# Kernel tuning notes

Hardware: AMD Instinct MI355X
Metric: run time of the kernel (lower is better)

Reference implementation:

```python
import jax, jax.numpy as jnp
import numpy as np
import math

D_MODEL = 1024
H = 16
D_K = D_MODEL // H
D_FF = 4096
NEG = -1e9


def layer_norm(x, alpha, bias):
    # Faithful to source: mean over last dim, UNBIASED std (torch.std default),
    # eps defined in source but never used in forward.
    mean = jnp.mean(x, axis=-1, keepdims=True)
    std = jnp.std(x, axis=-1, ddof=1, keepdims=True)
    return (x - mean) / std * alpha + bias


def mha(x, mask, w_q, w_k, w_v, w_o):
    B, S, D = x.shape
    q = (x @ w_q.T).reshape(B, S, H, D_K)
    k = (x @ w_k.T).reshape(B, S, H, D_K)
    v = (x @ w_v.T).reshape(B, S, H, D_K)
    scores = jnp.einsum('bqhd,bkhd->bhqk', q, k) / math.sqrt(D_K)
    scores = jnp.where(mask, NEG, scores)
    attn = jax.nn.softmax(scores, axis=-1)
    out = jnp.einsum('bhqk,bkhd->bqhd', attn, v).reshape(B, S, D)
    return out @ w_o.T


def setup_inputs() -> dict:
    key = jax.random.key(0)
    ks = jax.random.split(key, 16)
    B, S = 4, 2048
    s = 0.02
    return {
        'x': jax.random.normal(ks[0], (B, S, D_MODEL), jnp.float32),
        'w_q': jax.random.normal(ks[1], (D_MODEL, D_MODEL), jnp.float32) * s,
        'w_k': jax.random.normal(ks[2], (D_MODEL, D_MODEL), jnp.float32) * s,
        'w_v': jax.random.normal(ks[3], (D_MODEL, D_MODEL), jnp.float32) * s,
        'w_o': jax.random.normal(ks[4], (D_MODEL, D_MODEL), jnp.float32) * s,
        'l1_w': jax.random.normal(ks[5], (D_FF, D_MODEL), jnp.float32) * s,
        'l1_b': jnp.zeros((D_FF,), jnp.float32),
        'l2_w': jax.random.normal(ks[6], (D_MODEL, D_FF), jnp.float32) * s,
        'l2_b': jnp.zeros((D_MODEL,), jnp.float32),
        'norm1_a': jnp.ones((D_MODEL,), jnp.float32),
        'norm1_b': jnp.zeros((D_MODEL,), jnp.float32),
        'norm2_a': jnp.ones((D_MODEL,), jnp.float32),
        'norm2_b': jnp.zeros((D_MODEL,), jnp.float32),
        'normf_a': jnp.ones((D_MODEL,), jnp.float32),
        'normf_b': jnp.zeros((D_MODEL,), jnp.float32),
        'mask': jax.random.randint(ks[7], (B, 1, 1, S), 0, 2) == 1,
    }


def reference(x, w_q, w_k, w_v, w_o, l1_w, l1_b, l2_w, l2_b,
              norm1_a, norm1_b, norm2_a, norm2_b, normf_a, normf_b, mask):
    # residual 1: pre-norm self-attention (dropout is identity at eval)
    x = x + mha(layer_norm(x, norm1_a, norm1_b), mask, w_q, w_k, w_v, w_o)
    # residual 2: pre-norm FFN
    h = layer_norm(x, norm2_a, norm2_b)
    ff = jax.nn.relu(h @ l1_w.T + l1_b) @ l2_w.T + l2_b
    x = x + ff
    return layer_norm(x, normf_a, normf_b)
```

## Files before the change

kernel.cpp:

```cpp
#include <hip/hip_runtime.h>
#include <hip/hip_bf16.h>


typedef __bf16 bf16x8 __attribute__((ext_vector_type(8)));
typedef float f32x4 __attribute__((ext_vector_type(4)));
typedef unsigned short u16x8 __attribute__((ext_vector_type(8)));
using bf16 = __hip_bfloat16;

__device__ __forceinline__ f32x4 mfma16(bf16x8 a, bf16x8 b, f32x4 c) {
  return __builtin_amdgcn_mfma_f32_16x16x32_bf16(a, b, c, 0, 0, 0);
}

__device__ __forceinline__ int swz(int row, int blk) {
  return row * 64 + ((blk ^ (row & 7)) << 3);
}

__device__ __forceinline__ void stage_tile64(unsigned short* lds,
                                             const bf16* g, int ld, int rows) {
  const int lane = threadIdx.x & 63, wid = threadIdx.x >> 6;
  const int r8 = lane >> 3, blk = lane & 7;
  const bf16* gl = g + (size_t)r8 * ld + ((blk ^ r8) << 3);
  const int passes = rows >> 3;
  for (int p = wid; p < passes; p += 4) {
    __builtin_amdgcn_global_load_lds(
        (const __attribute__((address_space(1))) void*)(gl + (size_t)(p * 8) * ld),
        (__attribute__((address_space(3))) void*)(lds + p * 512),
        16, 0, 0);
  }
}

__device__ __forceinline__ short bfb(float x) {
  return (short)__hip_bfloat16_raw(__float2bfloat16(x)).x;
}

__global__ __launch_bounds__(256) void cvt_k(const float* __restrict__ s,
                                             bf16* __restrict__ d, int n) {
  const int i = (blockIdx.x * 256 + threadIdx.x) * 4;
  if (i + 3 < n) {
    const float4 v = *reinterpret_cast<const float4*>(s + i);
    ushort4 o;
    o.x = (unsigned short)bfb(v.x);
    o.y = (unsigned short)bfb(v.y);
    o.z = (unsigned short)bfb(v.z);
    o.w = (unsigned short)bfb(v.w);
    *reinterpret_cast<ushort4*>(d + i) = o;
  }
}

template <bool OUT_F32>
__global__ __launch_bounds__(256) void layernorm_k(const float* __restrict__ in,
                                                   const float* __restrict__ gamma,
                                                   const float* __restrict__ beta,
                                                   void* __restrict__ out) {
  __shared__ float red[8];
  const int row = blockIdx.x, t = threadIdx.x;
  const float4 vv = reinterpret_cast<const float4*>(in + (size_t)row * 1024)[t];
  const float x0 = vv.x, x1 = vv.y, x2 = vv.z, x3 = vv.w;
  float s = x0 + x1 + x2 + x3;
#pragma unroll
  for (int off = 32; off; off >>= 1) s += __shfl_down(s, off);
  if ((t & 63) == 0) red[t >> 6] = s;
  __syncthreads();
  const float mean = (red[0] + red[1] + red[2] + red[3]) * (1.0f / 1024.0f);
  const float d0 = x0 - mean, d1 = x1 - mean, d2 = x2 - mean, d3 = x3 - mean;
  float sq = d0 * d0 + d1 * d1 + d2 * d2 + d3 * d3;
#pragma unroll
  for (int off = 32; off; off >>= 1) sq += __shfl_down(sq, off);
  if ((t & 63) == 0) red[4 + (t >> 6)] = sq;
  __syncthreads();
  const float var =
      fmaxf((red[4] + red[5] + red[6] + red[7]) * (1.0f / 1023.0f), 1e-20f);
  const float rstd = rsqrtf(var);
  const float4 ga = reinterpret_cast<const float4*>(gamma)[t];
  const float4 be = reinterpret_cast<const float4*>(beta)[t];
  const float y0 = d0 * rstd * ga.x + be.x;
  const float y1 = d1 * rstd * ga.y + be.y;
  const float y2 = d2 * rstd * ga.z + be.z;
  const float y3 = d3 * rstd * ga.w + be.w;
  if (OUT_F32) {
    reinterpret_cast<float4*>((float*)out + (size_t)row * 1024)[t] =
        make_float4(y0, y1, y2, y3);
  } else {
    ushort4 o;
    o.x = (unsigned short)bfb(y0);
    o.y = (unsigned short)bfb(y1);
    o.z = (unsigned short)bfb(y2);
    o.w = (unsigned short)bfb(y3);
    reinterpret_cast<ushort4*>((bf16*)out + (size_t)row * 1024)[t] = o;
  }
}

template <bool HAS_BIAS, bool RELU, bool HAS_RES, bool OUT_F32>
__global__ __launch_bounds__(256) void gemm_bt(const bf16* __restrict__ A,
                                               const bf16* __restrict__ W,
                                               const float* __restrict__ bias,
                                               const float* __restrict__ resid,
                                               void* __restrict__ out,
                                               int M, int N, int K,
                                               int lda, int ldw) {
  __shared__ __align__(16) unsigned short As[128 * 64];
  __shared__ __align__(16) unsigned short Bs[128 * 64];
  const int lane = threadIdx.x & 63, wid = threadIdx.x >> 6;
  const int n16 = lane & 15, quad = lane >> 4;
  const int wm = (wid >> 1) * 64, wn = (wid & 1) * 64;
  const int tm = blockIdx.x * 128, tn = blockIdx.y * 128;
  f32x4 acc[4][4] = {};
  for (int k0 = 0; k0 < K; k0 += 64) {
    stage_tile64(As, A + (size_t)tm * lda + k0, lda, 128);
    stage_tile64(Bs, W + (size_t)tn * ldw + k0, ldw, 128);
    __syncthreads();
#pragma unroll
    for (int kk = 0; kk < 64; kk += 32) {
      bf16x8 af[4], bw[4];
#pragma unroll
      for (int i = 0; i < 4; ++i)
        af[i] = *reinterpret_cast<const bf16x8*>(
            &As[swz(wm + i * 16 + n16, (kk >> 3) + quad)]);
#pragma unroll
      for (int j = 0; j < 4; ++j)
        bw[j] = *reinterpret_cast<const bf16x8*>(
            &Bs[swz(wn + j * 16 + n16, (kk >> 3) + quad)]);
#pragma unroll
      for (int i = 0; i < 4; ++i)
#pragma unroll
        for (int j = 0; j < 4; ++j) acc[i][j] = mfma16(af[i], bw[j], acc[i][j]);
    }
    __syncthreads();
  }
#pragma unroll
  for (int i = 0; i < 4; ++i) {
#pragma unroll
    for (int j = 0; j < 4; ++j) {
      const int n = tn + wn + j * 16 + n16;
      const float bv = HAS_BIAS ? bias[n] : 0.0f;
#pragma unroll
      for (int r = 0; r < 4; ++r) {
        const int m = tm + wm + i * 16 + quad * 4 + r;
        float vv = acc[i][j][r] + bv;
        if (RELU) vv = fmaxf(vv, 0.0f);
        if (HAS_RES) vv += resid[(size_t)m * N + n];
        if (OUT_F32)
          ((float*)out)[(size_t)m * N + n] = vv;
        else
          ((bf16*)out)[(size_t)m * N + n] = __float2bfloat16(vv);
      }
    }
  }
}

__global__ void detect_mask_k(const unsigned int* __restrict__ m,
                              int* __restrict__ flag) {
  __shared__ int s;
  if (threadIdx.x == 0) s = 0;
  __syncthreads();
  unsigned int acc = 0;
  for (int i = threadIdx.x; i < 512; i += 256) acc |= m[i] & 0xFFFFFF00u;
  if (acc) atomicOr(&s, 1);
  __syncthreads();
  if (threadIdx.x == 0) *flag = s;
}

__global__ __launch_bounds__(256) void prep_mask_k(const int* __restrict__ m,
                                                   const int* __restrict__ flag,
                                                   float* __restrict__ mf,
                                                   int n) {
  const int i = blockIdx.x * 256 + threadIdx.x;
  if (i < n) {
    const int v = (*flag) ? (int)((const unsigned char*)m)[i] : m[i];
    mf[i] = v ? -1e9f : 0.0f;
  }
}

__global__ __launch_bounds__(256) void attn_k(const bf16* __restrict__ q,
                                              const bf16* __restrict__ kmat,
                                              const bf16* __restrict__ v,
                                              const float* __restrict__ maskf,
                                              bf16* __restrict__ out, int BHN) {
  __shared__ __align__(16) unsigned short Ks[64 * 64];
  __shared__ __align__(16) unsigned short Vs[64 * 72];
  const int lane = threadIdx.x & 63, wid = threadIdx.x >> 6;
  const int n16 = lane & 15, quad = lane >> 4;
  const int bid = blockIdx.x;
  const int bh = bid % BHN, qb = bid / BHN;
  const int b = bh >> 4, h = bh & 15;
  const size_t bhoff = (size_t)b * 2048 * 1024 + h * 64;
  const float* mfb = maskf + b * 2048;
  const int qrow0 = qb * 128 + wid * 32;

  bf16x8 qf[2][2];
#pragma unroll
  for (int g = 0; g < 2; ++g) {
    const bf16* qp = q + bhoff + (size_t)(qrow0 + g * 16 + n16) * 1024 + quad * 8;
    qf[g][0] = *reinterpret_cast<const bf16x8*>(qp);
    qf[g][1] = *reinterpret_cast<const bf16x8*>(qp + 32);
  }
  bf16x8 ones;
#pragma unroll
  for (int e = 0; e < 8; ++e) ones[e] = (__bf16)1.0f;
  f32x4 oacc[2][4] = {};
  f32x4 lacc[2] = {};
  const int prow = ((n16 >> 2) << 3) + (n16 & 3);

  for (int kt = 0; kt < 2048; kt += 64) {
    stage_tile64(Ks, kmat + bhoff + (size_t)kt * 1024, 1024, 64);
    {
      const int key = lane, dc = wid * 16;
      const bf16* vp = v + bhoff + (size_t)(kt + key) * 1024 + dc;
      const u16x8 a = *reinterpret_cast<const u16x8*>(vp);
      const u16x8 bq = *reinterpret_cast<const u16x8*>(vp + 8);
#pragma unroll
      for (int e = 0; e < 8; ++e) {
        Vs[(dc + e) * 72 + key] = a[e];
        Vs[(dc + 8 + e) * 72 + key] = bq[e];
      }
    }
    __syncthreads();
#pragma unroll
    for (int sub = 0; sub < 2; ++sub) {
      const int kb = sub * 32;
      bf16x8 aflo[2], afhi[2];
#pragma unroll
      for (int st = 0; st < 2; ++st) {
        const int row = kb + prow + st * 4;
        aflo[st] = *reinterpret_cast<const bf16x8*>(&Ks[swz(row, quad)]);
        afhi[st] = *reinterpret_cast<const bf16x8*>(&Ks[swz(row, 4 + quad)]);
      }
      f32x4 z[2][2];
#pragma unroll
      for (int g = 0; g < 2; ++g)
#pragma unroll
        for (int st = 0; st < 2; ++st) {
          f32x4 zz = {};
          zz = mfma16(aflo[st], qf[g][0], zz);
          zz = mfma16(afhi[st], qf[g][1], zz);
          z[g][st] = zz;
        }
      const float4 m0 =
          *reinterpret_cast<const float4*>(mfb + kt + kb + quad * 8);
      const float4 m1 =
          *reinterpret_cast<const float4*>(mfb + kt + kb + quad * 8 + 4);
      bf16x8 vf[4];
#pragma unroll
      for (int j = 0; j < 4; ++j)
        vf[j] = *reinterpret_cast<const bf16x8*>(
            &Vs[(j * 16 + n16) * 72 + kb + quad * 8]);
#pragma unroll
      for (int g = 0; g < 2; ++g) {
        bf16x8 pf;
#pragma unroll
        for (int r = 0; r < 4; ++r) {
          const float e0 =
              __expf(fmaf(z[g][0][r], 0.125f, ((const float*)&m0)[r]));
          const float e1 =
              __expf(fmaf(z[g][1][r], 0.125f, ((const float*)&m1)[r]));
          pf[r] = (__bf16)e0;
          pf[4 + r] = (__bf16)e1;
        }
#pragma unroll
        for (int j = 0; j < 4; ++j) oacc[g][j] = mfma16(pf, vf[j], oacc[g][j]);
        lacc[g] = mfma16(pf, ones, lacc[g]);
      }
    }
    __syncthreads();
  }
#pragma unroll
  for (int g = 0; g < 2; ++g) {
#pragma unroll
    for (int r = 0; r < 4; ++r) {
      const float lr = 1.0f / fmaxf(lacc[g][r], 1e-20f);
      bf16* op = out + bhoff + (size_t)(qrow0 + g * 16 + quad * 4 + r) * 1024;
#pragma unroll
      for (int j = 0; j < 4; ++j)
        op[j * 16 + n16] = __float2bfloat16(oacc[g][j][r] * lr);
    }
  }
}

extern "C" void kernel_launch(void* const* d_in, const int* in_sizes, int n_in,
                              void* d_out, int out_size, void* d_ws,
                              size_t ws_size, hipStream_t stream) {
  const float* x    = (const float*)d_in[0];
  const float* w_q  = (const float*)d_in[1];
  const float* w_k  = (const float*)d_in[2];
  const float* w_v  = (const float*)d_in[3];
  const float* w_o  = (const float*)d_in[4];
  const float* l1_w = (const float*)d_in[5];
  const float* l1_b = (const float*)d_in[6];
  const float* l2_w = (const float*)d_in[7];
  const float* l2_b = (const float*)d_in[8];
  const float* n1a  = (const float*)d_in[9];
  const float* n1b  = (const float*)d_in[10];
  const float* n2a  = (const float*)d_in[11];
  const float* n2b  = (const float*)d_in[12];
  const float* nfa  = (const float*)d_in[13];
  const float* nfb  = (const float*)d_in[14];
  const int* mask   = (const int*)d_in[15];

  const int D = 1024, FF = 4096;
  const int M = in_sizes[0] / D;

  const size_t MB = 1024ull * 1024ull;
  if (ws_size < 121 * MB) return;
  char* w = (char*)d_ws;
  bf16* WQ  = (bf16*)(w + 0 * MB);
  bf16* WK  = (bf16*)(w + 2 * MB);
  bf16* WV  = (bf16*)(w + 4 * MB);
  bf16* WO  = (bf16*)(w + 6 * MB);
  bf16* L1W = (bf16*)(w + 8 * MB);
  bf16* L2W = (bf16*)(w + 16 * MB);
  bf16* LN1 = (bf16*)(w + 24 * MB);
  bf16* Qb  = (bf16*)(w + 40 * MB);
  bf16* Kb  = (bf16*)(w + 56 * MB);
  bf16* Vb  = (bf16*)(w + 72 * MB);
  bf16* ATT = LN1;
  bf16* HLN = Qb;
  bf16* FF1 = Kb;
  float* X1 = (float*)(w + 88 * MB);
  int* FLAG = (int*)(w + 120 * MB);
  float* MASKF = (float*)(w + 120 * MB + 256);

  const dim3 blk(256);
  cvt_k<<<dim3(D * D / 1024), blk, 0, stream>>>(w_q, WQ, D * D);
  cvt_k<<<dim3(D * D / 1024), blk, 0, stream>>>(w_k, WK, D * D);
  cvt_k<<<dim3(D * D / 1024), blk, 0, stream>>>(w_v, WV, D * D);
  cvt_k<<<dim3(D * D / 1024), blk, 0, stream>>>(w_o, WO, D * D);
  cvt_k<<<dim3(FF * D / 1024), blk, 0, stream>>>(l1_w, L1W, FF * D);
  cvt_k<<<dim3(FF * D / 1024), blk, 0, stream>>>(l2_w, L2W, FF * D);
  detect_mask_k<<<1, blk, 0, stream>>>((const unsigned int*)mask, FLAG);
  prep_mask_k<<<dim3((M + 255) / 256), blk, 0, stream>>>(mask, FLAG, MASKF, M);

  layernorm_k<false><<<M, blk, 0, stream>>>(x, n1a, n1b, LN1);
  gemm_bt<false, false, false, false><<<dim3(M / 128, D / 128), blk, 0, stream>>>(
      LN1, WQ, nullptr, nullptr, Qb, M, D, D, D, D);
  gemm_bt<false, false, false, false><<<dim3(M / 128, D / 128), blk, 0, stream>>>(
      LN1, WK, nullptr, nullptr, Kb, M, D, D, D, D);
  gemm_bt<false, false, false, false><<<dim3(M / 128, D / 128), blk, 0, stream>>>(
      LN1, WV, nullptr, nullptr, Vb, M, D, D, D, D);
  const int BHN = (M / 2048) * 16;
  attn_k<<<dim3((M / 128) * 16), blk, 0, stream>>>(Qb, Kb, Vb, MASKF, ATT, BHN);
  gemm_bt<false, false, true, true><<<dim3(M / 128, D / 128), blk, 0, stream>>>(
      ATT, WO, nullptr, x, X1, M, D, D, D, D);
  layernorm_k<false><<<M, blk, 0, stream>>>(X1, n2a, n2b, HLN);
  for (int c = 0; c < 2; ++c) {
    gemm_bt<true, true, false, false>
        <<<dim3(M / 128, 2048 / 128), blk, 0, stream>>>(
            HLN, L1W + (size_t)c * 2048 * D, l1_b + c * 2048, nullptr, FF1, M,
            2048, D, D, D);
    if (c == 0)
      gemm_bt<true, false, true, true>
          <<<dim3(M / 128, D / 128), blk, 0, stream>>>(
              FF1, L2W + c * 2048, l2_b, X1, X1, M, D, 2048, 2048, FF);
    else
      gemm_bt<false, false, true, true>
          <<<dim3(M / 128, D / 128), blk, 0, stream>>>(
              FF1, L2W + c * 2048, nullptr, X1, X1, M, D, 2048, 2048, FF);
  }
  layernorm_k<true><<<M, blk, 0, stream>>>(X1, nfa, nfb, (float*)d_out);
}
```

Measured before the change: 578.3 us.

## Fuse QKV GEMM, double-buffer attention K/V tiles, use exp2 softmax, merge mask kernels

Concatenates the Q, K and V weights so a single GEMM writes an interleaved QKV buffer, and the attention kernel reads it with a row stride of 3072. The attention loop now double-buffers K and V tiles in LDS, prefetching the next tile while computing on the current one, and drops one barrier per iteration. The softmax uses exp2 with a log2e-scaled multiplier and mask value. Mask detection and preparation are merged into one kernel. The aim is fewer launches, better GEMM occupancy and hiding global-load latency in attention, at the cost of double the LDS and some extra registers.

```diff
diff --git a/kernel.cpp b/kernel.cpp
--- a/kernel.cpp
+++ b/kernel.cpp
@@ -148,49 +148,46 @@
   }
 }
 
-__global__ void detect_mask_k(const unsigned int* __restrict__ m,
-                              int* __restrict__ flag) {
+__global__ __launch_bounds__(256) void prep_mask_k(const int* __restrict__ m,
+                                                   float* __restrict__ mf,
+                                                   int n) {
   __shared__ int s;
   if (threadIdx.x == 0) s = 0;
   __syncthreads();
   unsigned int acc = 0;
-  for (int i = threadIdx.x; i < 512; i += 256) acc |= m[i] & 0xFFFFFF00u;
+  for (int i = threadIdx.x; i < 512; i += 256)
+    acc |= ((const unsigned int*)m)[i] & 0xFFFFFF00u;
   if (acc) atomicOr(&s, 1);
   __syncthreads();
-  if (threadIdx.x == 0) *flag = s;
-}
-
-__global__ __launch_bounds__(256) void prep_mask_k(const int* __restrict__ m,
-                                                   const int* __restrict__ flag,
-                                                   float* __restrict__ mf,
-                                                   int n) {
+  const bool bytes = (s != 0);
   const int i = blockIdx.x * 256 + threadIdx.x;
   if (i < n) {
-    const int v = (*flag) ? (int)((const unsigned char*)m)[i] : m[i];
-    mf[i] = v ? -1e9f : 0.0f;
-  }
-}
-
-__global__ __launch_bounds__(256) void attn_k(const bf16* __restrict__ q,
-                                              const bf16* __restrict__ kmat,
-                                              const bf16* __restrict__ v,
+    const int v = bytes ? (int)((const unsigned char*)m)[i] : m[i];
+    mf[i] = v ? -1.4427e9f : 0.0f;
+  }
+}
+
+__global__ __launch_bounds__(256) void attn_k(const bf16* __restrict__ qkv,
                                               const float* __restrict__ maskf,
                                               bf16* __restrict__ out, int BHN) {
-  __shared__ __align__(16) unsigned short Ks[64 * 64];
-  __shared__ __align__(16) unsigned short Vs[64 * 72];
+  __shared__ __align__(16) unsigned short Ks[2][64 * 64];
+  __shared__ __align__(16) unsigned short Vs[2][64 * 72];
   const int lane = threadIdx.x & 63, wid = threadIdx.x >> 6;
   const int n16 = lane & 15, quad = lane >> 4;
   const int bid = blockIdx.x;
   const int bh = bid % BHN, qb = bid / BHN;
   const int b = bh >> 4, h = bh & 15;
-  const size_t bhoff = (size_t)b * 2048 * 1024 + h * 64;
+  const size_t rowb = (size_t)b * 2048 * 3072;
+  const bf16* qp0 = qkv + rowb + h * 64;
+  const bf16* kp0 = qkv + rowb + 1024 + h * 64;
+  const bf16* vp0 = qkv + rowb + 2048 + h * 64;
   const float* mfb = maskf + b * 2048;
   const int qrow0 = qb * 128 + wid * 32;
 
   bf16x8 qf[2][2];
 #pragma unroll
   for (int g = 0; g < 2; ++g) {
-    const bf16* qp = q + bhoff + (size_t)(qrow0 + g * 16 + n16) * 1024 + quad * 8;
+    const bf16* qp = qp0 + (size_t)(qrow0 + g * 16 + n16) * 3072 + quad * 8;
     qf[g][0] = *reinterpret_cast<const bf16x8*>(qp);
     qf[g][1] = *reinterpret_cast<const bf16x8*>(qp + 32);
   }
@@ -200,21 +197,32 @@
   f32x4 oacc[2][4] = {};
   f32x4 lacc[2] = {};
   const int prow = ((n16 >> 2) << 3) + (n16 & 3);
-
+  const int vkey = lane, vdc = wid * 16;
+
+  stage_tile64(Ks[0], kp0, 3072, 64);
+  {
+    const bf16* vp = vp0 + (size_t)vkey * 3072 + vdc;
+    const u16x8 a = *reinterpret_cast<const u16x8*>(vp);
+    const u16x8 bq = *reinterpret_cast<const u16x8*>(vp + 8);
+#pragma unroll
+    for (int e = 0; e < 8; ++e) {
+      Vs[0][(vdc + e) * 72 + vkey] = a[e];
+      Vs[0][(vdc + 8 + e) * 72 + vkey] = bq[e];
+    }
+  }
+  int cur = 0;
   for (int kt = 0; kt < 2048; kt += 64) {
-    stage_tile64(Ks, kmat + bhoff + (size_t)kt * 1024, 1024, 64);
-    {
-      const int key = lane, dc = wid * 16;
-      const bf16* vp = v + bhoff + (size_t)(kt + key) * 1024 + dc;
-      const u16x8 a = *reinterpret_cast<const u16x8*>(vp);
-      const u16x8 bq = *reinterpret_cast<const u16x8*>(vp + 8);
-#pragma unroll
-      for (int e = 0; e < 8; ++e) {
-        Vs[(dc + e) * 72 + key] = a[e];
-        Vs[(dc + 8 + e) * 72 + key] = bq[e];
-      }
-    }
     __syncthreads();
+    const bool hasNext = (kt + 64 < 2048);
+    u16x8 na = {}, nb = {};
+    if (hasNext) {
+      stage_tile64(Ks[cur ^ 1], kp0 + (size_t)(kt + 64) * 3072, 3072, 64);
+      const bf16* vp = vp0 + (size_t)(kt + 64 + vkey) * 3072 + vdc;
+      na = *reinterpret_cast<const u16x8*>(vp);
+      nb = *reinterpret_cast<const u16x8*>(vp + 8);
+    }
+    const unsigned short* Kc = Ks[cur];
+    const unsigned short* Vc = Vs[cur];
 #pragma unroll
     for (int sub = 0; sub < 2; ++sub) {
       const int kb = sub * 32;
@@ -222,8 +230,8 @@
 #pragma unroll
       for (int st = 0; st < 2; ++st) {
         const int row = kb + prow + st * 4;
-        aflo[st] = *reinterpret_cast<const bf16x8*>(&Ks[swz(row, quad)]);
-        afhi[st] = *reinterpret_cast<const bf16x8*>(&Ks[swz(row, 4 + quad)]);
+        aflo[st] = *reinterpret_cast<const bf16x8*>(&Kc[swz(row, quad)]);
+        afhi[st] = *reinterpret_cast<const bf16x8*>(&Kc[swz(row, 4 + quad)]);
       }
       f32x4 z[2][2];
 #pragma unroll
@@ -243,16 +251,16 @@
 #pragma unroll
       for (int j = 0; j < 4; ++j)
         vf[j] = *reinterpret_cast<const bf16x8*>(
-            &Vs[(j * 16 + n16) * 72 + kb + quad * 8]);
+            &Vc[(j * 16 + n16) * 72 + kb + quad * 8]);
 #pragma unroll
       for (int g = 0; g < 2; ++g) {
         bf16x8 pf;
 #pragma unroll
         for (int r = 0; r < 4; ++r) {
-          const float e0 =
-              __expf(fmaf(z[g][0][r], 0.125f, ((const float*)&m0)[r]));
-          const float e1 =
-              __expf(fmaf(z[g][1][r], 0.125f, ((const float*)&m1)[r]));
+          const float e0 = __builtin_amdgcn_exp2f(
+              fmaf(z[g][0][r], 0.18033688f, ((const float*)&m0)[r]));
+          const float e1 = __builtin_amdgcn_exp2f(
+              fmaf(z[g][1][r], 0.18033688f, ((const float*)&m1)[r]));
           pf[r] = (__bf16)e0;
           pf[4 + r] = (__bf16)e1;
         }
@@ -261,14 +269,24 @@
         lacc[g] = mfma16(pf, ones, lacc[g]);
       }
     }
-    __syncthreads();
+    if (hasNext) {
+      unsigned short* Vn = Vs[cur ^ 1];
+#pragma unroll
+      for (int e = 0; e < 8; ++e) {
+        Vn[(vdc + e) * 72 + vkey] = na[e];
+        Vn[(vdc + 8 + e) * 72 + vkey] = nb[e];
+      }
+    }
+    cur ^= 1;
   }
 #pragma unroll
   for (int g = 0; g < 2; ++g) {
 #pragma unroll
     for (int r = 0; r < 4; ++r) {
       const float lr = 1.0f / fmaxf(lacc[g][r], 1e-20f);
-      bf16* op = out + bhoff + (size_t)(qrow0 + g * 16 + quad * 4 + r) * 1024;
+      bf16* op =
+          out + (size_t)(b * 2048 + qrow0 + g * 16 + quad * 4 + r) * 1024 +
+          h * 64;
 #pragma unroll
       for (int j = 0; j < 4; ++j)
         op[j * 16 + n16] = __float2bfloat16(oacc[g][j][r] * lr);
@@ -302,42 +320,34 @@
   const size_t MB = 1024ull * 1024ull;
   if (ws_size < 121 * MB) return;
   char* w = (char*)d_ws;
-  bf16* WQ  = (bf16*)(w + 0 * MB);
-  bf16* WK  = (bf16*)(w + 2 * MB);
-  bf16* WV  = (bf16*)(w + 4 * MB);
-  bf16* WO  = (bf16*)(w + 6 * MB);
-  bf16* L1W = (bf16*)(w + 8 * MB);
-  bf16* L2W = (bf16*)(w + 16 * MB);
-  bf16* LN1 = (bf16*)(w + 24 * MB);
-  bf16* Qb  = (bf16*)(w + 40 * MB);
-  bf16* Kb  = (bf16*)(w + 56 * MB);
-  bf16* Vb  = (bf16*)(w + 72 * MB);
-  bf16* ATT = LN1;
-  bf16* HLN = Qb;
-  bf16* FF1 = Kb;
-  float* X1 = (float*)(w + 88 * MB);
-  int* FLAG = (int*)(w + 120 * MB);
-  float* MASKF = (float*)(w + 120 * MB + 256);
+  bf16* WQKV = (bf16*)(w + 0 * MB);
+  bf16* WO   = (bf16*)(w + 6 * MB);
+  bf16* L1W  = (bf16*)(w + 8 * MB);
+  bf16* L2W  = (bf16*)(w + 16 * MB);
+  bf16* LN1  = (bf16*)(w + 24 * MB);
+  bf16* QKV  = (bf16*)(w + 40 * MB);
+  bf16* ATT  = LN1;
+  bf16* HLN  = (bf16*)(w + 40 * MB);
+  bf16* FF1  = (bf16*)(w + 56 * MB);
+  float* X1  = (float*)(w + 88 * MB);
+  float* MASKF = (float*)(w + 120 * MB);
 
   const dim3 blk(256);
-  cvt_k<<<dim3(D * D / 1024), blk, 0, stream>>>(w_q, WQ, D * D);
-  cvt_k<<<dim3(D * D / 1024), blk, 0, stream>>>(w_k, WK, D * D);
-  cvt_k<<<dim3(D * D / 1024), blk, 0, stream>>>(w_v, WV, D * D);
+  cvt_k<<<dim3(D * D / 1024), blk, 0, stream>>>(w_q, WQKV, D * D);
+  cvt_k<<<dim3(D * D / 1024), blk, 0, stream>>>(w_k, WQKV + D * D, D * D);
+  cvt_k<<<dim3(D * D / 1024), blk, 0, stream>>>(w_v, WQKV + 2 * D * D, D * D);
   cvt_k<<<dim3(D * D / 1024), blk, 0, stream>>>(w_o, WO, D * D);
   cvt_k<<<dim3(FF * D / 1024), blk, 0, stream>>>(l1_w, L1W, FF * D);
   cvt_k<<<dim3(FF * D / 1024), blk, 0, stream>>>(l2_w, L2W, FF * D);
-  detect_mask_k<<<1, blk, 0, stream>>>((const unsigned int*)mask, FLAG);
-  prep_mask_k<<<dim3((M + 255) / 256), blk, 0, stream>>>(mask, FLAG, MASKF, M);
+  prep_mask_k<<<dim3((M + 255) / 256), blk, 0, stream>>>(mask, MASKF, M);
 
   layernorm_k<false><<<M, blk, 0, stream>>>(x, n1a, n1b, LN1);
-  gemm_bt<false, false, false, false><<<dim3(M / 128, D / 128), blk, 0, stream>>>(
-      LN1, WQ, nullptr, nullptr, Qb, M, D, D, D, D);
-  gemm_bt<false, false, false, false><<<dim3(M / 128, D / 128), blk, 0, stream>>>(
-      LN1, WK, nullptr, nullptr, Kb, M, D, D, D, D);
-  gemm_bt<false, false, false, false><<<dim3(M / 128, D / 128), blk, 0, stream>>>(
-      LN1, WV, nullptr, nullptr, Vb, M, D, D, D, D);
+  gemm_bt<false, false, false, false>
+      <<<dim3(M / 128, 3072 / 128), blk, 0, stream>>>(LN1, WQKV, nullptr,
+                                                      nullptr, QKV, M, 3072, D,
+                                                      D, D);
   const int BHN = (M / 2048) * 16;
-  attn_k<<<dim3((M / 128) * 16), blk, 0, stream>>>(Qb, Kb, Vb, MASKF, ATT, BHN);
+  attn_k<<<dim3((M / 128) * 16), blk, 0, stream>>>(QKV, MASKF, ATT, BHN);
   gemm_bt<false, false, true, true><<<dim3(M / 128, D / 128), blk, 0, stream>>>(
       ATT, WO, nullptr, x, X1, M, D, D, D, D);
   layernorm_k<false><<<M, blk, 0, stream>>>(X1, n2a, n2b, HLN);
```

New measurement: 569.0 us. Within noise of the previous version (-1.6%).
